# Kernel optimization log

Hardware: AMD Instinct MI355X
Metric: run time of the kernel (lower is better)

Reference implementation:

```python
import jax, jax.numpy as jnp
import numpy as np

B, L, D, H = 2, 2048, 1024, 16
HD = D // H  # head_dim = 64


def setup_inputs() -> dict:
    key = jax.random.key(0)
    ks = jax.random.split(key, 8)
    queries = jax.random.normal(ks[0], (B, L, D), dtype=jnp.float32)
    keys = jax.random.normal(ks[1], (B, L, D), dtype=jnp.float32)
    values = jax.random.normal(ks[2], (B, L, D), dtype=jnp.float32)
    mask = jax.random.randint(ks[3], (B, L, L), 0, 2) > 0  # True = masked
    s = 1.0 / np.sqrt(D)
    W_q = jax.random.normal(ks[4], (D, D), dtype=jnp.float32) * s
    W_k = jax.random.normal(ks[5], (D, D), dtype=jnp.float32) * s
    W_v = jax.random.normal(ks[6], (D, D), dtype=jnp.float32) * s
    W_o = jax.random.normal(ks[7], (D, D), dtype=jnp.float32) * s
    return {"queries": queries, "keys": keys, "values": values,
            "W_q": W_q, "W_k": W_k, "W_v": W_v, "W_o": W_o, "mask": mask}


def _split_heads(x):
    # [B, L, D] -> [B, H, L, HD]
    return x.reshape(B, L, H, HD).transpose(0, 2, 1, 3)


def reference(queries, keys, values, W_q, W_k, W_v, W_o, mask):
    # Linear projections (nn.Linear: x @ W.T, no bias)
    q = _split_heads(queries @ W_q.T)   # [B,H,Lq,HD]
    k = _split_heads(keys @ W_k.T)      # [B,H,Lk,HD]
    v = _split_heads(values @ W_v.T)    # [B,H,Lk,HD]
    scores = jnp.einsum('bnqd,bnkd->bnqk', q, k) / np.sqrt(HD)
    scores = jnp.where(mask[:, None, :, :], -1e9, scores)
    attn = jax.nn.softmax(scores, axis=-1)
    ctx = jnp.einsum('bnqk,bnkd->bnqd', attn, v)
    ctx = ctx.transpose(0, 2, 1, 3).reshape(B, L, D)
    return ctx @ W_o.T  # dropout p=0.0 -> identity
```

## Files before the change

### kernel.cpp

```cpp
#include <hip/hip_runtime.h>
#include <hip/hip_bf16.h>

typedef __bf16 bf16;
typedef __attribute__((ext_vector_type(8))) __bf16 bf16x8;
typedef __attribute__((ext_vector_type(4))) __bf16 bf16x4;
typedef __attribute__((ext_vector_type(4))) float f32x4;

#define B_   2
#define L_   2048
#define D_   1024
#define H_   16
#define HD_  64

__device__ __forceinline__ float fast_exp2(float x) {
  float e; asm("v_exp_f32 %0, %1" : "=v"(e) : "v"(x)); return e;
}

__device__ __forceinline__ void gll16(const bf16* g, bf16* l) {
  __builtin_amdgcn_global_load_lds((const __attribute__((address_space(1))) void*)g,
                                   (__attribute__((address_space(3))) void*)l,
                                   16, 0, 0);
}

__global__ void detect_kernel(const unsigned short* __restrict__ q_u,
                              const unsigned char* __restrict__ m_u,
                              int* __restrict__ flags) {
  __shared__ int cnt, odd;
  if (threadIdx.x == 0) { cnt = 0; odd = 0; }
  __syncthreads();
  int c = 0, o = 0;
  for (int i = 0; i < 8; i++) {
    int idx = threadIdx.x * 8 + i;
    unsigned e = (q_u[idx] >> 7) & 0xFF;
    if (e >= 0x8F || (e > 0 && e <= 0x6F)) c++;
    if ((idx & 3) && m_u[idx]) o = 1;
  }
  atomicAdd(&cnt, c);
  if (o) atomicOr(&odd, 1);
  __syncthreads();
  if (threadIdx.x == 0) { flags[0] = (cnt > 128) ? 1 : 0; flags[1] = odd; }
}

__device__ __forceinline__ void canon_body(const void* src, bf16* dst, int i, int f) {
  if (f) {
    const float4* s = (const float4*)src;
    float4 a = s[i / 4], b2 = s[i / 4 + 1];
    bf16x8 o;
    o[0] = (bf16)a.x;  o[1] = (bf16)a.y;  o[2] = (bf16)a.z;  o[3] = (bf16)a.w;
    o[4] = (bf16)b2.x; o[5] = (bf16)b2.y; o[6] = (bf16)b2.z; o[7] = (bf16)b2.w;
    *(bf16x8*)(dst + i) = o;
  } else {
    *(bf16x8*)(dst + i) = ((const bf16x8*)src)[i / 8];
  }
}

__global__ __launch_bounds__(256) void canon_pack(
    const void* xq, const void* xk, const void* xv,
    const void* Wq, const void* Wk, const void* Wv, const void* Wo,
    const void* mp,
    bf16* cxq, bf16* cxk, bf16* cxv,
    bf16* cWq, bf16* cWk, bf16* cWv, bf16* cWo,
    unsigned* __restrict__ bitsT,
    const int* __restrict__ flags) {
  int t = blockIdx.x;
  if (t >= 8192) {
    int wid = (t - 8192) * 256 + threadIdx.x;
    unsigned v = 0;
    if (flags[1]) {
      const uchar4* p = (const uchar4*)mp;
#pragma unroll
      for (int c = 0; c < 8; c++) {
        uchar4 u = p[wid * 8 + c];
        v |= (u.x ? 1u : 0u) << (c * 4 + 0);
        v |= (u.y ? 1u : 0u) << (c * 4 + 1);
        v |= (u.z ? 1u : 0u) << (c * 4 + 2);
        v |= (u.w ? 1u : 0u) << (c * 4 + 3);
      }
    } else {
      const int4* p = (const int4*)mp;
#pragma unroll
      for (int c = 0; c < 8; c++) {
        int4 u = p[wid * 8 + c];
        v |= (u.x ? 1u : 0u) << (c * 4 + 0);
        v |= (u.y ? 1u : 0u) << (c * 4 + 1);
        v |= (u.z ? 1u : 0u) << (c * 4 + 2);
        v |= (u.w ? 1u : 0u) << (c * 4 + 3);
      }
    }
    int row = wid >> 6, word = wid & 63;
    int kt = word >> 1, half = word & 1;
    bitsT[((size_t)kt * 4096 + row) * 2 + half] = v;
    return;
  }
  const int f = flags[0];
  const void* src; bf16* dst; int base;
  if (t < 2048)      { src = xq; dst = cxq; base = t * 2048; }
  else if (t < 4096) { src = xk; dst = cxk; base = (t - 2048) * 2048; }
  else if (t < 6144) { src = xv; dst = cxv; base = (t - 4096) * 2048; }
  else {
    int w = t - 6144, wi = w >> 9;
    base = (w & 511) * 2048;
    if (wi == 0)      { src = Wq; dst = cWq; }
    else if (wi == 1) { src = Wk; dst = cWk; }
    else if (wi == 2) { src = Wv; dst = cWv; }
    else              { src = Wo; dst = cWo; }
  }
  canon_body(src, dst, base + threadIdx.x * 8, f);
}

__global__ __launch_bounds__(256) void gemm_qkv(
    const bf16* __restrict__ Aq, const bf16* __restrict__ Bq, bf16* __restrict__ Cq,
    const bf16* __restrict__ Ak, const bf16* __restrict__ Bk, bf16* __restrict__ Ck,
    const bf16* __restrict__ Av, const bf16* __restrict__ Bv, bf16* __restrict__ VT) {
  __shared__ bf16 smem[128 * 136];
  bf16* sA = smem;
  bf16* sB = smem + 4096;
  const int z = blockIdx.z;
  const bf16* A  = (z == 0) ? Aq : (z == 1) ? Ak : Av;
  const bf16* Bm = (z == 0) ? Bq : (z == 1) ? Bk : Bv;

  const int tid = threadIdx.x;
  const int w = tid >> 6, lane = tid & 63, qd = lane >> 4, r = lane & 15;
  const int wm = w >> 1, wn = w & 1;
  const int m0 = blockIdx.x * 128, n0 = blockIdx.y * 128;

  f32x4 acc[4][4];
#pragma unroll
  for (int i = 0; i < 4; i++)
#pragma unroll
    for (int j = 0; j < 4; j++) acc[i][j] = (f32x4){0.f, 0.f, 0.f, 0.f};

  for (int k0 = 0; k0 < 1024; k0 += 32) {
    __syncthreads();
#pragma unroll
    for (int p = 0; p < 2; p++) {
      int c = p * 256 + tid;
      gll16(A + (size_t)(m0 + (c >> 2)) * 1024 + k0 + (c & 3) * 8, sA + c * 8);
    }
#pragma unroll
    for (int p = 0; p < 2; p++) {
      int c = p * 256 + tid;
      gll16(Bm + (size_t)(n0 + (c >> 2)) * 1024 + k0 + (c & 3) * 8, sB + c * 8);
    }
    __syncthreads();
    bf16x8 af[4], bfv[4];
#pragma unroll
    for (int i = 0; i < 4; i++)
      af[i] = *(const bf16x8*)&sA[(wm * 64 + i * 16 + r) * 32 + qd * 8];
#pragma unroll
    for (int j = 0; j < 4; j++)
      bfv[j] = *(const bf16x8*)&sB[(wn * 64 + j * 16 + r) * 32 + qd * 8];
#pragma unroll
    for (int i = 0; i < 4; i++)
#pragma unroll
      for (int j = 0; j < 4; j++)
        acc[i][j] = __builtin_amdgcn_mfma_f32_16x16x32_bf16(af[i], bfv[j], acc[i][j], 0, 0, 0);
  }

  if (z < 2) {
    bf16* C = (z == 0) ? Cq : Ck;
    const float s = (z == 0) ? 0.1803368801f : 1.0f;
#pragma unroll
    for (int i = 0; i < 4; i++)
#pragma unroll
      for (int j = 0; j < 4; j++)
#pragma unroll
        for (int rr = 0; rr < 4; rr++) {
          int row = m0 + wm * 64 + i * 16 + qd * 4 + rr;
          int col = n0 + wn * 64 + j * 16 + r;
          C[(size_t)row * 1024 + col] = (bf16)(acc[i][j][rr] * s);
        }
  } else {
    __syncthreads();
#pragma unroll
    for (int i = 0; i < 4; i++)
#pragma unroll
      for (int j = 0; j < 4; j++) {
        int col = wn * 64 + j * 16 + r;
        int rowb = wm * 64 + i * 16 + qd * 4;
        bf16x4 v4;
#pragma unroll
        for (int rr = 0; rr < 4; rr++) v4[rr] = (bf16)acc[i][j][rr];
        *(bf16x4*)&smem[col * 136 + rowb] = v4;
      }
    __syncthreads();
    const int b = m0 >> 11, tok0 = m0 & 2047, h0 = n0 >> 6;
#pragma unroll
    for (int p = 0; p < 8; p++) {
      int c = p * 256 + tid;
      int dl = c >> 4, ch = c & 15;
      bf16x8 v = *(const bf16x8*)&smem[dl * 136 + ch * 8];
      int head = h0 + (dl >> 6), d = dl & 63;
      *(bf16x8*)(VT + ((size_t)((b * 16 + head) * 64 + d)) * 2048 + tok0 + ch * 8) = v;
    }
  }
}

__global__ __launch_bounds__(256) void gemm_nt_out(const bf16* __restrict__ A,
                                                   const bf16* __restrict__ Bm,
                                                   void* __restrict__ Cout,
                                                   const int* __restrict__ flags) {
  __shared__ bf16 sA[128 * 32];
  __shared__ bf16 sB[64 * 32];
  const int tid = threadIdx.x;
  const int w = tid >> 6, lane = tid & 63, qd = lane >> 4, r = lane & 15;
  const int wm = w >> 1, wn = w & 1;
  const int m0 = blockIdx.x * 128, n0 = blockIdx.y * 64;

  f32x4 acc[4][2];
#pragma unroll
  for (int i = 0; i < 4; i++)
#pragma unroll
    for (int j = 0; j < 2; j++) acc[i][j] = (f32x4){0.f, 0.f, 0.f, 0.f};

  for (int k0 = 0; k0 < 1024; k0 += 32) {
    __syncthreads();
    {
      int c0 = tid;
      gll16(A + (size_t)(m0 + (c0 >> 2)) * 1024 + k0 + (c0 & 3) * 8, sA + c0 * 8);
      int c1 = 256 + tid;
      gll16(A + (size_t)(m0 + (c1 >> 2)) * 1024 + k0 + (c1 & 3) * 8, sA + c1 * 8);
      int cb = tid;
      gll16(Bm + (size_t)(n0 + (cb >> 2)) * 1024 + k0 + (cb & 3) * 8, sB + cb * 8);
    }
    __syncthreads();
    bf16x8 af[4], bfv[2];
#pragma unroll
    for (int i = 0; i < 4; i++)
      af[i] = *(const bf16x8*)&sA[(wm * 64 + i * 16 + r) * 32 + qd * 8];
#pragma unroll
    for (int j = 0; j < 2; j++)
      bfv[j] = *(const bf16x8*)&sB[(wn * 32 + j * 16 + r) * 32 + qd * 8];
#pragma unroll
    for (int i = 0; i < 4; i++)
#pragma unroll
      for (int j = 0; j < 2; j++)
        acc[i][j] = __builtin_amdgcn_mfma_f32_16x16x32_bf16(af[i], bfv[j], acc[i][j], 0, 0, 0);
  }
  const int f = flags[0];
#pragma unroll
  for (int i = 0; i < 4; i++)
#pragma unroll
    for (int j = 0; j < 2; j++)
#pragma unroll
      for (int rr = 0; rr < 4; rr++) {
        int row = m0 + wm * 64 + i * 16 + qd * 4 + rr;
        int col = n0 + wn * 32 + j * 16 + r;
        if (f) ((float*)Cout)[(size_t)row * 1024 + col] = acc[i][j][rr];
        else   ((bf16*)Cout)[(size_t)row * 1024 + col] = (bf16)acc[i][j][rr];
      }
}

__global__ __launch_bounds__(256) void attn_kernel(const bf16* __restrict__ Q,
                                                   const bf16* __restrict__ Kp,
                                                   const bf16* __restrict__ Vt,
                                                   const unsigned* __restrict__ bitsT,
                                                   bf16* __restrict__ OP,
                                                   float* __restrict__ LP) {
  __shared__ bf16 sK[64 * 64];
  __shared__ bf16 sVT[64 * 64];
  __shared__ bf16 sP[128 * 72];
  const int tid = threadIdx.x;
  const int w = tid >> 6, lane = tid & 63, qd = lane >> 4, r = lane & 15;
  const int bh = blockIdx.y, b = bh >> 4, h = bh & 15;
  const int q0 = blockIdx.x * 128;
  const int z = blockIdx.z;

  bf16x8 qf[2][2];
#pragma unroll
  for (int i = 0; i < 2; i++)
#pragma unroll
    for (int ks = 0; ks < 2; ks++)
      qf[i][ks] = *(const bf16x8*)(Q + (size_t)(b * L_ + q0 + w * 32 + i * 16 + r) * D_ +
                                   h * HD_ + ks * 32 + qd * 8);

  bf16x8 ones;
#pragma unroll
  for (int e = 0; e < 8; e++) ones[e] = (bf16)1.0f;

  f32x4 o[2][4], lacc[2];
#pragma unroll
  for (int i = 0; i < 2; i++) {
#pragma unroll
    for (int dj = 0; dj < 4; dj++) o[i][dj] = (f32x4){0.f, 0.f, 0.f, 0.f};
    lacc[i] = (f32x4){0.f, 0.f, 0.f, 0.f};
  }

  for (int kt = z * 16; kt < z * 16 + 16; kt++) {
    __syncthreads();
#pragma unroll
    for (int p = 0; p < 2; p++) {
      int c = p * 256 + tid;
      int row = c >> 3, kc = c & 7;
      int kcg = kc ^ (row & 7);
      gll16(Kp + (size_t)(b * L_ + kt * 64 + row) * D_ + h * HD_ + kcg * 8, sK + c * 8);
    }
#pragma unroll
    for (int p = 0; p < 2; p++) {
      int c = p * 256 + tid;
      int row = c >> 3, kc = c & 7;
      int kcg = kc ^ (row & 7);
      gll16(Vt + (size_t)(bh * 64 + row) * L_ + kt * 64 + kcg * 8, sVT + c * 8);
    }

    uint2 m64[2];
#pragma unroll
    for (int i = 0; i < 2; i++)
      m64[i] = *(const uint2*)(bitsT +
          ((size_t)kt * 4096 + b * 2048 + q0 + w * 32 + i * 16 + r) * 2);

    __syncthreads();

    bf16x8 kf[4][2];
#pragma unroll
    for (int j = 0; j < 4; j++)
#pragma unroll
      for (int ks = 0; ks < 2; ks++) {
        int row = j * 16 + r;
        int phys = (ks * 4 + qd) ^ (row & 7);
        kf[j][ks] = *(const bf16x8*)&sK[row * 64 + phys * 8];
      }

#pragma unroll
    for (int i = 0; i < 2; i++) {
      f32x4 S[4];
#pragma unroll
      for (int j = 0; j < 4; j++) {
        S[j] = (f32x4){0.f, 0.f, 0.f, 0.f};
#pragma unroll
        for (int ks = 0; ks < 2; ks++)
          S[j] = __builtin_amdgcn_mfma_f32_16x16x32_bf16(kf[j][ks], qf[i][ks], S[j], 0, 0, 0);
      }
#pragma unroll
      for (int j = 0; j < 4; j++) {
        unsigned word = (j < 2) ? m64[i].x : m64[i].y;
        unsigned nib = (word >> ((j & 1) * 16 + qd * 4)) & 0xFu;
        bf16x4 pv;
#pragma unroll
        for (int rr = 0; rr < 4; rr++) {
          float e = fast_exp2(S[j][rr]);
          pv[rr] = (bf16)(((nib >> rr) & 1u) ? 0.f : e);
        }
        *(bf16x4*)&sP[(w * 32 + i * 16 + r) * 72 + j * 16 + qd * 4] = pv;
      }
    }
    asm volatile("s_waitcnt lgkmcnt(0)" ::: "memory");

    bf16x8 vf[4][2];
#pragma unroll
    for (int dj = 0; dj < 4; dj++)
#pragma unroll
      for (int ks = 0; ks < 2; ks++) {
        int row = dj * 16 + r;
        int phys = (ks * 4 + qd) ^ (row & 7);
        vf[dj][ks] = *(const bf16x8*)&sVT[row * 64 + phys * 8];
      }
#pragma unroll
    for (int i = 0; i < 2; i++)
#pragma unroll
      for (int ks = 0; ks < 2; ks++) {
        bf16x8 pf = *(const bf16x8*)&sP[(w * 32 + i * 16 + r) * 72 + ks * 32 + qd * 8];
#pragma unroll
        for (int dj = 0; dj < 4; dj++)
          o[i][dj] = __builtin_amdgcn_mfma_f32_16x16x32_bf16(pf, vf[dj][ks], o[i][dj], 0, 0, 0);
        lacc[i] = __builtin_amdgcn_mfma_f32_16x16x32_bf16(pf, ones, lacc[i], 0, 0, 0);
      }
  }

#pragma unroll
  for (int i = 0; i < 2; i++) {
#pragma unroll
    for (int dj = 0; dj < 4; dj++)
#pragma unroll
      for (int rr = 0; rr < 4; rr++) {
        int rg = b * L_ + q0 + w * 32 + i * 16 + qd * 4 + rr;
        int col = h * HD_ + dj * 16 + r;
        OP[((size_t)z * 4096 + rg) * 1024 + col] = (bf16)o[i][dj][rr];
      }
    if (r == 0) {
#pragma unroll
      for (int rr = 0; rr < 4; rr++) {
        int rg = b * L_ + q0 + w * 32 + i * 16 + qd * 4 + rr;
        LP[((size_t)z * 4096 + rg) * 16 + h] = lacc[i][rr];
      }
    }
  }
}

__global__ __launch_bounds__(256) void combine_kernel(const bf16* __restrict__ OP,
                                                      const float* __restrict__ LP,
                                                      bf16* __restrict__ CTX) {
  size_t idx = ((size_t)blockIdx.x * 256 + threadIdx.x) * 8;
  int row = (int)(idx >> 10), col = (int)(idx & 1023);
  bf16x8 a = *(const bf16x8*)(OP + idx);
  bf16x8 c = *(const bf16x8*)(OP + (size_t)4096 * 1024 + idx);
  int h = col >> 6;
  float l = LP[row * 16 + h] + LP[65536 + row * 16 + h];
  float inv = 1.0f / l;
  bf16x8 o;
#pragma unroll
  for (int e = 0; e < 8; e++) o[e] = (bf16)(((float)a[e] + (float)c[e]) * inv);
  *(bf16x8*)(CTX + idx) = o;
}

extern "C" void kernel_launch(void* const* d_in, const int* in_sizes, int n_in,
                              void* d_out, int out_size, void* d_ws, size_t ws_size,
                              hipStream_t stream) {
  const void* xq = d_in[0];
  const void* xk = d_in[1];
  const void* xv = d_in[2];
  const void* Wq = d_in[3];
  const void* Wk = d_in[4];
  const void* Wv = d_in[5];
  const void* Wo = d_in[6];
  const void* mask = d_in[7];

  char* ws = (char*)d_ws;
  const size_t MB = 1048576;
  int*      FLAGS = (int*)(ws + 0);
  unsigned* BITS  = (unsigned*)(ws + 4096);
  bf16* cWo = (bf16*)(ws + 2 * MB);
  bf16* cWq = (bf16*)(ws + 4 * MB);
  bf16* cWk = (bf16*)(ws + 6 * MB);
  bf16* cWv = (bf16*)(ws + 8 * MB);
  bf16* cxq = (bf16*)(ws + 10 * MB);
  bf16* cxk = (bf16*)(ws + 18 * MB);
  bf16* cxv = (bf16*)(ws + 26 * MB);
  bf16* Q   = (bf16*)(ws + 34 * MB);
  bf16* K   = (bf16*)(ws + 42 * MB);
  bf16* VT  = (bf16*)(ws + 50 * MB);
  bf16*  OP  = (bf16*)(ws + 4 * MB);
  float* LP  = (float*)(ws + 20 * MB);
  bf16*  CTX = (bf16*)(ws + 26 * MB);

  detect_kernel<<<1, 256, 0, stream>>>((const unsigned short*)xq,
                                       (const unsigned char*)mask, FLAGS);
  canon_pack<<<9216, 256, 0, stream>>>(xq, xk, xv, Wq, Wk, Wv, Wo, mask,
                                       cxq, cxk, cxv, cWq, cWk, cWv, cWo,
                                       BITS, FLAGS);
  gemm_qkv<<<dim3(32, 8, 3), 256, 0, stream>>>(cxq, cWq, Q,
                                               cxk, cWk, K,
                                               cxv, cWv, VT);
  attn_kernel<<<dim3(16, 32, 2), 256, 0, stream>>>(Q, K, VT, BITS, OP, LP);
  combine_kernel<<<2048, 256, 0, stream>>>(OP, LP, CTX);
  gemm_nt_out<<<dim3(32, 16), 256, 0, stream>>>(CTX, cWo, d_out, FLAGS);
}
```

Before: 269.1 us.

## Double-buffer K/V tiles in attention kernel and prefetch next tile's mask

Splits the K and V^T shared-memory tiles into two buffers. The next tile's global-to-LDS loads and mask-bit loads are issued before the current tile is computed, with an explicit vmcnt wait, so memory latency overlaps the MFMA and softmax work. It also raises wave priority around the MFMA blocks. The cost is double the LDS for K/V, which may lower occupancy, and the hand-set vmcnt counts are fragile.

```diff
diff --git a/kernel.cpp b/kernel.cpp
--- a/kernel.cpp
+++ b/kernel.cpp
@@ -257,8 +257,8 @@
                                                    const unsigned* __restrict__ bitsT,
                                                    bf16* __restrict__ OP,
                                                    float* __restrict__ LP) {
-  __shared__ bf16 sK[64 * 64];
-  __shared__ bf16 sVT[64 * 64];
+  __shared__ bf16 sK[2][64 * 64];
+  __shared__ bf16 sVT[2][64 * 64];
   __shared__ bf16 sP[128 * 72];
   const int tid = threadIdx.x;
   const int w = tid >> 6, lane = tid & 63, qd = lane >> 4, r = lane & 15;
@@ -286,30 +286,51 @@
     lacc[i] = (f32x4){0.f, 0.f, 0.f, 0.f};
   }
 
-  for (int kt = z * 16; kt < z * 16 + 16; kt++) {
-    __syncthreads();
-#pragma unroll
-    for (int p = 0; p < 2; p++) {
-      int c = p * 256 + tid;
-      int row = c >> 3, kc = c & 7;
-      int kcg = kc ^ (row & 7);
-      gll16(Kp + (size_t)(b * L_ + kt * 64 + row) * D_ + h * HD_ + kcg * 8, sK + c * 8);
-    }
-#pragma unroll
-    for (int p = 0; p < 2; p++) {
-      int c = p * 256 + tid;
-      int row = c >> 3, kc = c & 7;
-      int kcg = kc ^ (row & 7);
-      gll16(Vt + (size_t)(bh * 64 + row) * L_ + kt * 64 + kcg * 8, sVT + c * 8);
-    }
-
-    uint2 m64[2];
-#pragma unroll
-    for (int i = 0; i < 2; i++)
-      m64[i] = *(const uint2*)(bitsT +
-          ((size_t)kt * 4096 + b * 2048 + q0 + w * 32 + i * 16 + r) * 2);
-
-    __syncthreads();
+#define STAGE_KV(KT, KB, VB)                                                        \
+  {                                                                                 \
+    _Pragma("unroll")                                                               \
+    for (int p = 0; p < 2; p++) {                                                   \
+      int c = p * 256 + tid;                                                        \
+      int row = c >> 3, kc = c & 7;                                                 \
+      int kcg = kc ^ (row & 7);                                                     \
+      gll16(Kp + (size_t)(b * L_ + (KT) * 64 + row) * D_ + h * HD_ + kcg * 8,       \
+            (KB) + c * 8);                                                          \
+    }                                                                               \
+    _Pragma("unroll")                                                               \
+    for (int p = 0; p < 2; p++) {                                                   \
+      int c = p * 256 + tid;                                                        \
+      int row = c >> 3, kc = c & 7;                                                 \
+      int kcg = kc ^ (row & 7);                                                     \
+      gll16(Vt + (size_t)(bh * 64 + row) * L_ + (KT) * 64 + kcg * 8, (VB) + c * 8); \
+    }                                                                               \
+  }
+
+#define MLOAD(KT, M0, M1)                                                                       \
+  {                                                                                             \
+    M0 = *(const uint2*)(bitsT + ((size_t)(KT) * 4096 + b * 2048 + q0 + w * 32 + r) * 2);       \
+    M1 = *(const uint2*)(bitsT + ((size_t)(KT) * 4096 + b * 2048 + q0 + w * 32 + 16 + r) * 2);  \
+  }
+
+  const int kt0 = z * 16;
+  STAGE_KV(kt0, &sK[0][0], &sVT[0][0]);
+  uint2 mc0, mc1, mn0, mn1;
+  MLOAD(kt0, mc0, mc1);
+  mn0 = mc0; mn1 = mc1;
+
+  for (int it = 0; it < 16; ++it) {
+    const int kt = kt0 + it;
+    const bf16* kb = &sK[it & 1][0];
+    const bf16* vb = &sVT[it & 1][0];
+
+    if (it < 15) {
+      STAGE_KV(kt + 1, &sK[(it + 1) & 1][0], &sVT[(it + 1) & 1][0]);
+      MLOAD(kt + 1, mn0, mn1);
+      asm volatile("s_waitcnt vmcnt(6)" ::: "memory");
+    } else {
+      asm volatile("s_waitcnt vmcnt(0)" ::: "memory");
+    }
+    __builtin_amdgcn_sched_barrier(0);
+    __builtin_amdgcn_s_barrier();
 
     bf16x8 kf[4][2];
 #pragma unroll
@@ -318,12 +339,13 @@
       for (int ks = 0; ks < 2; ks++) {
         int row = j * 16 + r;
         int phys = (ks * 4 + qd) ^ (row & 7);
-        kf[j][ks] = *(const bf16x8*)&sK[row * 64 + phys * 8];
+        kf[j][ks] = *(const bf16x8*)&kb[row * 64 + phys * 8];
       }
 
 #pragma unroll
     for (int i = 0; i < 2; i++) {
       f32x4 S[4];
+      __builtin_amdgcn_s_setprio(1);
 #pragma unroll
       for (int j = 0; j < 4; j++) {
         S[j] = (f32x4){0.f, 0.f, 0.f, 0.f};
@@ -331,9 +353,11 @@
         for (int ks = 0; ks < 2; ks++)
           S[j] = __builtin_amdgcn_mfma_f32_16x16x32_bf16(kf[j][ks], qf[i][ks], S[j], 0, 0, 0);
       }
+      __builtin_amdgcn_s_setprio(0);
+      const uint2 m64 = (i == 0) ? mc0 : mc1;
 #pragma unroll
       for (int j = 0; j < 4; j++) {
-        unsigned word = (j < 2) ? m64[i].x : m64[i].y;
+        unsigned word = (j < 2) ? m64.x : m64.y;
         unsigned nib = (word >> ((j & 1) * 16 + qd * 4)) & 0xFu;
         bf16x4 pv;
 #pragma unroll
@@ -353,8 +377,9 @@
       for (int ks = 0; ks < 2; ks++) {
         int row = dj * 16 + r;
         int phys = (ks * 4 + qd) ^ (row & 7);
-        vf[dj][ks] = *(const bf16x8*)&sVT[row * 64 + phys * 8];
-      }
+        vf[dj][ks] = *(const bf16x8*)&vb[row * 64 + phys * 8];
+      }
+    __builtin_amdgcn_s_setprio(1);
 #pragma unroll
     for (int i = 0; i < 2; i++)
 #pragma unroll
@@ -365,7 +390,13 @@
           o[i][dj] = __builtin_amdgcn_mfma_f32_16x16x32_bf16(pf, vf[dj][ks], o[i][dj], 0, 0, 0);
         lacc[i] = __builtin_amdgcn_mfma_f32_16x16x32_bf16(pf, ones, lacc[i], 0, 0, 0);
       }
-  }
+    __builtin_amdgcn_s_setprio(0);
+
+    __builtin_amdgcn_s_barrier();
+    mc0 = mn0; mc1 = mn1;
+  }
+#undef STAGE_KV
+#undef MLOAD
 
 #pragma unroll
   for (int i = 0; i < 2; i++) {
```

New measurement: 269.2 us. Within noise of the previous version (+0.0%).
